# Performance work log

Measured on AMD Instinct MI355X. Metric: run time of the kernel, lower is better.

The kernel has to match this reference:

```python
import jax, jax.numpy as jnp
import numpy as np

N, H = 65536, 256
RHO_REF = 1000.0
MOMENTUM_W, CONTINUITY_W = 1.0, 10.0


def setup_inputs() -> dict:
    key = jax.random.key(0)
    ks = jax.random.split(key, 6)
    sc = lambda k, shape, fan_in: jax.random.normal(k, shape, jnp.float32) * (1.0 / fan_in) ** 0.5
    return {
        "sample_points": jax.random.normal(ks[0], (N, 3), jnp.float32),
        "sample_times": jax.random.uniform(ks[1], (N, 1), jnp.float32),
        "viscosity": jax.random.uniform(ks[2], (N,), jnp.float32) * 1e-3 + 1e-6,
        "W1": sc(ks[3], (4, H), 4),
        "b1": jnp.zeros((H,), jnp.float32),
        "W2": sc(ks[4], (H, H), H),
        "b2": jnp.zeros((H,), jnp.float32),
        "W3": sc(ks[5], (H, 5), H),
        "b3": jnp.zeros((5,), jnp.float32),
    }


def reference(sample_points, sample_times, viscosity, W1, b1, W2, b2, W3, b3):
    gravity = jnp.array([0.0, -9.81, 0.0], dtype=sample_points.dtype)

    def mlp(z):  # z: (4,) = (x, y, zcoord, t) -> (5,) = (ux, uy, uz, p, rho_raw)
        h = jnp.tanh(z @ W1 + b1)
        h = jnp.tanh(h @ W2 + b2)
        return h @ W3 + b3

    def up_fn(z):  # (ux, uy, uz, p)
        return mlp(z)[:4]

    def u_fn(z):  # (ux, uy, uz)
        return mlp(z)[:3]

    def per_point(z):
        out = mlp(z)
        u = out[:3]
        rho = RHO_REF * (1.0 + 0.1 * jnp.tanh(out[4]))
        J = jax.jacfwd(up_fn)(z)                      # (4,4): d[u,p]/d[x,y,z,t]
        Hs = jax.jacfwd(jax.jacfwd(u_fn))(z)          # (3,4,4): second derivs of u
        lap = Hs[:, 0, 0] + Hs[:, 1, 1] + Hs[:, 2, 2]  # (3,) spatial Laplacian of u
        return u, rho, J, lap

    z = jnp.concatenate([sample_points, sample_times], axis=1)  # (N,4)
    u, rho, J, lap = jax.vmap(per_point)(z)

    du_dt = J[:, :3, 3]                                # (N,3)
    conv = jnp.einsum('nj,nij->ni', u, J[:, :3, :3])   # (u . grad) u
    grad_p = J[:, 3, :3]                               # (N,3)
    R = du_dt + conv + grad_p / rho[:, None] - viscosity[:, None] * lap - gravity[None, :]
    R_cont = J[:, 0, 0] + J[:, 1, 1] + J[:, 2, 2]      # div u

    momentum_loss = (R ** 2).mean(axis=0).sum()
    continuity_loss = (R_cont ** 2).mean()
    total = MOMENTUM_W * momentum_loss + CONTINUITY_W * continuity_loss
    return jnp.stack([total, momentum_loss, continuity_loss])
```

## Files before the change

kernel.cpp:

```cpp
#include <hip/hip_runtime.h>


#define NPTS 65536
#define BP   16
#define NBLK (NPTS / BP)
#define KPAD 264
#define W3T_OFF 135168
#define PART_OFF 143360

typedef short s16x8 __attribute__((ext_vector_type(8)));
typedef float f32x4 __attribute__((ext_vector_type(4)));

static __device__ __forceinline__ unsigned short f2bf(float f){
  unsigned int u = __float_as_uint(f);
  u = (u + 0x7FFFu + ((u >> 16) & 1u)) >> 16;
  return (unsigned short)u;
}
static __device__ __forceinline__ unsigned cvtpk_bf16(float lo, float hi){
  unsigned r;
  asm("v_cvt_pk_bf16_f32 %0, %1, %2" : "=v"(r) : "v"(lo), "v"(hi));
  return r;
}
static __device__ __forceinline__ float fast_tanh(float x){
  float e = exp2f(x * 2.8853900817779268f);
  return 1.f - 2.f * __builtin_amdgcn_rcpf(e + 1.f);
}

__global__ void prep_w2t(const float* __restrict__ W2, unsigned short* __restrict__ w2t){
  int k = blockIdx.x, j = threadIdx.x;
  w2t[j * KPAD + k] = f2bf(W2[k * 256 + j]);
}

__global__ void prep_w3t(const float* __restrict__ W3, unsigned short* __restrict__ w3t){
  int idx = blockIdx.x * 256 + threadIdx.x;
  int n = idx >> 8, k = idx & 255;
  w3t[n * 256 + k] = (n < 5) ? f2bf(W3[k * 5 + n]) : (unsigned short)0;
}

__launch_bounds__(512, 4)
__global__ void ns_main(const float* __restrict__ pts, const float* __restrict__ times,
                        const float* __restrict__ visc,
                        const float* __restrict__ W1, const float* __restrict__ b1,
                        const float* __restrict__ b2, const float* __restrict__ b3,
                        const unsigned short* __restrict__ w2t,
                        const unsigned short* __restrict__ w3t,
                        float* __restrict__ parts){
  __shared__ __align__(16) unsigned char sA[128 * 512];

  const int t   = threadIdx.x;
  const int blk = blockIdx.x;

  {
    int p  = t >> 5;
    int jo = (t & 31) << 3;
    int n  = blk * BP + p;
    float z0 = pts[n*3+0], z1 = pts[n*3+1], z2 = pts[n*3+2], z3 = times[n];
    float w0v[8], w1v[8], w2v[8], w3v[8], bv[8];
    *(float4*)(w0v)   = *(const float4*)(W1 + jo);
    *(float4*)(w0v+4) = *(const float4*)(W1 + jo + 4);
    *(float4*)(w1v)   = *(const float4*)(W1 + 256 + jo);
    *(float4*)(w1v+4) = *(const float4*)(W1 + 256 + jo + 4);
    *(float4*)(w2v)   = *(const float4*)(W1 + 512 + jo);
    *(float4*)(w2v+4) = *(const float4*)(W1 + 512 + jo + 4);
    *(float4*)(w3v)   = *(const float4*)(W1 + 768 + jo);
    *(float4*)(w3v+4) = *(const float4*)(W1 + 768 + jo + 4);
    *(float4*)(bv)    = *(const float4*)(b1 + jo);
    *(float4*)(bv+4)  = *(const float4*)(b1 + jo + 4);
    float cv[8][8];
    #pragma unroll
    for (int jj = 0; jj < 8; ++jj){
      float w0 = w0v[jj], w1 = w1v[jj], w2 = w2v[jj], w3 = w3v[jj];
      float a  = bv[jj] + z0*w0 + z1*w1 + z2*w2 + z3*w3;
      float th = fast_tanh(a);
      float s  = 1.f - th*th;
      float m2 = -2.f * th * s;
      cv[0][jj] = th;
      cv[1][jj] = s*w0; cv[2][jj] = s*w1; cv[3][jj] = s*w2; cv[4][jj] = s*w3;
      cv[5][jj] = m2*w0*w0; cv[6][jj] = m2*w1*w1; cv[7][jj] = m2*w2*w2;
    }
    #pragma unroll
    for (int c = 0; c < 8; ++c){
      int row = ((p & 8) << 3) + ((c & 4) << 3) + ((p & 7) << 2) + (c & 3);
      int off = row*512 + ((jo << 1) ^ ((row & 7) << 4));
      uint4 v;
      v.x = cvtpk_bf16(cv[c][0], cv[c][1]);
      v.y = cvtpk_bf16(cv[c][2], cv[c][3]);
      v.z = cvtpk_bf16(cv[c][4], cv[c][5]);
      v.w = cvtpk_bf16(cv[c][6], cv[c][7]);
      *(uint4*)(sA + off) = v;
    }
  }
  __syncthreads();

  const int wid = t >> 6, lane = t & 63;
  const int g = lane >> 4, r16 = lane & 15;
  const int wr = wid >> 2, wc = wid & 3;
  const int xorv = (r16 & 7) << 4;

  f32x4 acc[4][4];
  #pragma unroll
  for (int a = 0; a < 4; ++a)
    #pragma unroll
    for (int b = 0; b < 4; ++b)
      acc[a][b] = (f32x4){0.f, 0.f, 0.f, 0.f};

  {
    const unsigned char* w2tB = (const unsigned char*)w2t;
    int abase0 = (wr*64 + r16)*512;
    const unsigned char* bptr[4];
    #pragma unroll
    for (int nt = 0; nt < 4; ++nt)
      bptr[nt] = w2tB + (((wc*64 + nt*16 + r16)*KPAD + g*8) << 1);
    #pragma unroll
    for (int ks = 0; ks < 8; ++ks){
      int k0 = ks * 32;
      int X  = ((k0 << 1) + (g << 4)) ^ xorv;
      s16x8 af[4], bfr[4];
      #pragma unroll
      for (int mt = 0; mt < 4; ++mt)
        af[mt] = *(const s16x8*)(sA + abase0 + mt*8192 + X);
      #pragma unroll
      for (int nt = 0; nt < 4; ++nt)
        bfr[nt] = *(const s16x8*)(bptr[nt] + (k0 << 1));
      #pragma unroll
      for (int mt = 0; mt < 4; ++mt)
        #pragma unroll
        for (int nt = 0; nt < 4; ++nt)
          acc[mt][nt] = __builtin_amdgcn_mfma_f32_16x16x32_bf16(af[mt], bfr[nt], acc[mt][nt], 0, 0, 0);
    }
  }
  __syncthreads();

  {
    float b2c[4];
    #pragma unroll
    for (int nt = 0; nt < 4; ++nt) b2c[nt] = b2[wc*64 + nt*16 + r16];
    int wadr[4][4];
    #pragma unroll
    for (int nt = 0; nt < 4; ++nt){
      int colb = (wc*64 + nt*16 + r16) << 1;
      #pragma unroll
      for (int c3 = 0; c3 < 4; ++c3)
        wadr[nt][c3] = (wr*64 + g*4 + c3)*512 + (colb ^ ((((g & 1) << 2) + c3) << 4));
    }
    #pragma unroll
    for (int mt = 0; mt < 2; ++mt){
      #pragma unroll
      for (int nt = 0; nt < 4; ++nt){
        f32x4 v = acc[mt][nt];
        f32x4 w = acc[mt+2][nt];
        float gv = fast_tanh(v[0] + b2c[nt]);
        float s2 = 1.f - gv*gv;
        float t2 = -2.f * gv * s2;
        float r0 = gv,      r1 = s2*v[1], r2 = s2*v[2], r3 = s2*v[3];
        float r4 = s2*w[0];
        float r5 = fmaf(t2*v[1], v[1], s2*w[1]);
        float r6 = fmaf(t2*v[2], v[2], s2*w[2]);
        float r7 = fmaf(t2*v[3], v[3], s2*w[3]);
        unsigned u;
        u = cvtpk_bf16(r0, r4);
        *(unsigned short*)(sA + wadr[nt][0] + mt*8192)         = (unsigned short)u;
        *(unsigned short*)(sA + wadr[nt][0] + mt*8192 + 16384) = (unsigned short)(u >> 16);
        u = cvtpk_bf16(r1, r5);
        *(unsigned short*)(sA + wadr[nt][1] + mt*8192)         = (unsigned short)u;
        *(unsigned short*)(sA + wadr[nt][1] + mt*8192 + 16384) = (unsigned short)(u >> 16);
        u = cvtpk_bf16(r2, r6);
        *(unsigned short*)(sA + wadr[nt][2] + mt*8192)         = (unsigned short)u;
        *(unsigned short*)(sA + wadr[nt][2] + mt*8192 + 16384) = (unsigned short)(u >> 16);
        u = cvtpk_bf16(r3, r7);
        *(unsigned short*)(sA + wadr[nt][3] + mt*8192)         = (unsigned short)u;
        *(unsigned short*)(sA + wadr[nt][3] + mt*8192 + 16384) = (unsigned short)(u >> 16);
      }
    }
  }
  __syncthreads();

  {
    f32x4 acc3 = (f32x4){0.f, 0.f, 0.f, 0.f};
    int rbase = (wid*16 + r16)*512;
    const unsigned char* w3tB = (const unsigned char*)w3t + ((r16*256 + g*8) << 1);
    #pragma unroll
    for (int ks = 0; ks < 8; ++ks){
      int k0 = ks * 32;
      int X  = ((k0 << 1) + (g << 4)) ^ xorv;
      s16x8 a3  = *(const s16x8*)(sA + rbase + X);
      s16x8 b3f = *(const s16x8*)(w3tB + (k0 << 1));
      acc3 = __builtin_amdgcn_mfma_f32_16x16x32_bf16(a3, b3f, acc3, 0, 0, 0);
    }
    if (r16 < 5){
      #pragma unroll
      for (int q = 0; q < 4; ++q){
        int row = wid*16 + g*4 + q;
        *(float*)(sA + row*512 + ((r16 << 2) ^ ((row & 7) << 4))) = acc3[q];
      }
    }
  }
  __syncthreads();

  float m_part = 0.f, c_part = 0.f;
  if (t < 16){
    int p = t, n = blk*BP + p;
    float o[8][5];
    #pragma unroll
    for (int c = 0; c < 8; ++c){
      int row = ((p & 8) << 3) + ((c & 4) << 3) + ((p & 7) << 2) + (c & 3);
      int swz = (row & 7) << 4;
      f32x4 v4 = *(const f32x4*)(sA + row*512 + swz);
      o[c][0] = v4[0]; o[c][1] = v4[1]; o[c][2] = v4[2]; o[c][3] = v4[3];
      o[c][4] = *(const float*)(sA + row*512 + (16 ^ swz));
    }
    #pragma unroll
    for (int m = 0; m < 5; ++m) o[0][m] += b3[m];

    float u0 = o[0][0], u1 = o[0][1], u2 = o[0][2];
    float rho = 1000.f * (1.f + 0.1f * fast_tanh(o[0][4]));
    float rr  = __builtin_amdgcn_rcpf(rho);
    float vis = visc[n];

    float conv0 = u0*o[1][0] + u1*o[2][0] + u2*o[3][0];
    float conv1 = u0*o[1][1] + u1*o[2][1] + u2*o[3][1];
    float conv2 = u0*o[1][2] + u1*o[2][2] + u2*o[3][2];
    float lap0 = o[5][0] + o[6][0] + o[7][0];
    float lap1 = o[5][1] + o[6][1] + o[7][1];
    float lap2 = o[5][2] + o[6][2] + o[7][2];
    float R0 = o[4][0] + conv0 + o[1][3]*rr - vis*lap0;
    float R1 = o[4][1] + conv1 + o[2][3]*rr - vis*lap1 + 9.81f;
    float R2 = o[4][2] + conv2 + o[3][3]*rr - vis*lap2;
    float Rc = o[1][0] + o[2][1] + o[3][2];

    m_part = R0*R0 + R1*R1 + R2*R2;
    c_part = Rc*Rc;
  }
  if (t < 64){
    #pragma unroll
    for (int off = 1; off < 16; off <<= 1){
      m_part += __shfl_xor(m_part, off, 64);
      c_part += __shfl_xor(c_part, off, 64);
    }
    if (t == 0){
      float2 pr; pr.x = m_part; pr.y = c_part;
      *(float2*)(parts + blk*2) = pr;
    }
  }
}

__global__ void ns_reduce(const float* __restrict__ parts, float* __restrict__ out){
  int t = threadIdx.x;
  float a = 0.f, b = 0.f;
  for (int i = t; i < NBLK; i += 256){ a += parts[2*i]; b += parts[2*i + 1]; }
  #pragma unroll
  for (int off = 32; off; off >>= 1){
    a += __shfl_down(a, off, 64);
    b += __shfl_down(b, off, 64);
  }
  __shared__ float sa[4], sb[4];
  int wid = t >> 6, lane = t & 63;
  if (lane == 0){ sa[wid] = a; sb[wid] = b; }
  __syncthreads();
  if (t == 0){
    float A = sa[0] + sa[1] + sa[2] + sa[3];
    float B = sb[0] + sb[1] + sb[2] + sb[3];
    float mom  = A / (float)NPTS;
    float cont = B / (float)NPTS;
    out[0] = mom + 10.f * cont;
    out[1] = mom;
    out[2] = cont;
  }
}

extern "C" void kernel_launch(void* const* d_in, const int* in_sizes, int n_in,
                              void* d_out, int out_size, void* d_ws, size_t ws_size,
                              hipStream_t stream) {
  const float* pts   = (const float*)d_in[0];
  const float* times = (const float*)d_in[1];
  const float* visc  = (const float*)d_in[2];
  const float* W1    = (const float*)d_in[3];
  const float* b1    = (const float*)d_in[4];
  const float* W2    = (const float*)d_in[5];
  const float* b2    = (const float*)d_in[6];
  const float* W3    = (const float*)d_in[7];
  const float* b3    = (const float*)d_in[8];
  float* out = (float*)d_out;

  unsigned short* w2t = (unsigned short*)d_ws;
  unsigned short* w3t = (unsigned short*)((char*)d_ws + W3T_OFF);
  float* parts        = (float*)((char*)d_ws + PART_OFF);

  prep_w2t<<<256, 256, 0, stream>>>(W2, w2t);
  prep_w3t<<<16, 256, 0, stream>>>(W3, w3t);
  ns_main<<<NBLK, 512, 0, stream>>>(pts, times, visc, W1, b1, b2, b3, w2t, w3t, parts);
  ns_reduce<<<1, 256, 0, stream>>>(parts, out);
}
```

Measured before the change: 135.6 us.

## Halve points per block to cut LDS and registers and raise occupancy

Each block now handles 8 points instead of 16. That halves the shared buffer to 32KB and the MFMA accumulator tile to 2x4, and the launch bound becomes 6 blocks per CU. Layer-1 work is spread as 4 columns per thread, and the row mapping, layer-2 writeback and final reduction are reworked to match. This aims for higher occupancy and less register pressure, but it doubles the block count and the W2 reads from global/L2 per point, and only half the waves do the layer-3 MFMA.

```diff
diff --git a/kernel.cpp b/kernel.cpp
--- a/kernel.cpp
+++ b/kernel.cpp
@@ -2,7 +2,7 @@
 
 
 #define NPTS 65536
-#define BP   16
+#define BP   8
 #define NBLK (NPTS / BP)
 #define KPAD 264
 #define W3T_OFF 135168
@@ -37,7 +37,7 @@
   w3t[n * 256 + k] = (n < 5) ? f2bf(W3[k * 5 + n]) : (unsigned short)0;
 }
 
-__launch_bounds__(512, 4)
+__launch_bounds__(512, 6)
 __global__ void ns_main(const float* __restrict__ pts, const float* __restrict__ times,
                         const float* __restrict__ visc,
                         const float* __restrict__ W1, const float* __restrict__ b1,
@@ -45,49 +45,54 @@
                         const unsigned short* __restrict__ w2t,
                         const unsigned short* __restrict__ w3t,
                         float* __restrict__ parts){
-  __shared__ __align__(16) unsigned char sA[128 * 512];
+  __shared__ __align__(16) unsigned char sA[64 * 512];
 
   const int t   = threadIdx.x;
   const int blk = blockIdx.x;
 
   {
-    int p  = t >> 5;
-    int jo = (t & 31) << 3;
+    int p  = t >> 6;
+    int jo = (t & 63) << 2;
     int n  = blk * BP + p;
     float z0 = pts[n*3+0], z1 = pts[n*3+1], z2 = pts[n*3+2], z3 = times[n];
-    float w0v[8], w1v[8], w2v[8], w3v[8], bv[8];
-    *(float4*)(w0v)   = *(const float4*)(W1 + jo);
-    *(float4*)(w0v+4) = *(const float4*)(W1 + jo + 4);
-    *(float4*)(w1v)   = *(const float4*)(W1 + 256 + jo);
-    *(float4*)(w1v+4) = *(const float4*)(W1 + 256 + jo + 4);
-    *(float4*)(w2v)   = *(const float4*)(W1 + 512 + jo);
-    *(float4*)(w2v+4) = *(const float4*)(W1 + 512 + jo + 4);
-    *(float4*)(w3v)   = *(const float4*)(W1 + 768 + jo);
-    *(float4*)(w3v+4) = *(const float4*)(W1 + 768 + jo + 4);
-    *(float4*)(bv)    = *(const float4*)(b1 + jo);
-    *(float4*)(bv+4)  = *(const float4*)(b1 + jo + 4);
-    float cv[8][8];
-    #pragma unroll
-    for (int jj = 0; jj < 8; ++jj){
-      float w0 = w0v[jj], w1 = w1v[jj], w2 = w2v[jj], w3 = w3v[jj];
-      float a  = bv[jj] + z0*w0 + z1*w1 + z2*w2 + z3*w3;
-      float th = fast_tanh(a);
-      float s  = 1.f - th*th;
-      float m2 = -2.f * th * s;
-      cv[0][jj] = th;
-      cv[1][jj] = s*w0; cv[2][jj] = s*w1; cv[3][jj] = s*w2; cv[4][jj] = s*w3;
-      cv[5][jj] = m2*w0*w0; cv[6][jj] = m2*w1*w1; cv[7][jj] = m2*w2*w2;
+    float4 wa = *(const float4*)(W1 + jo);
+    float4 wb = *(const float4*)(W1 + 256 + jo);
+    float4 wc4 = *(const float4*)(W1 + 512 + jo);
+    float4 wd = *(const float4*)(W1 + 768 + jo);
+    float4 bb = *(const float4*)(b1 + jo);
+    float th[4], sg[4], m2[4];
+    #pragma unroll
+    for (int jj = 0; jj < 4; ++jj){
+      float a = (&bb.x)[jj] + z0*(&wa.x)[jj] + z1*(&wb.x)[jj]
+                            + z2*(&wc4.x)[jj] + z3*(&wd.x)[jj];
+      float h = fast_tanh(a);
+      th[jj] = h;
+      sg[jj] = 1.f - h*h;
+      m2[jj] = -2.f * h * sg[jj];
     }
     #pragma unroll
     for (int c = 0; c < 8; ++c){
-      int row = ((p & 8) << 3) + ((c & 4) << 3) + ((p & 7) << 2) + (c & 3);
+      float x[4];
+      #pragma unroll
+      for (int jj = 0; jj < 4; ++jj){
+        float w0 = (&wa.x)[jj], w1 = (&wb.x)[jj], w2 = (&wc4.x)[jj];
+        float v;
+        if      (c == 0) v = th[jj];
+        else if (c == 1) v = sg[jj]*w0;
+        else if (c == 2) v = sg[jj]*w1;
+        else if (c == 3) v = sg[jj]*w2;
+        else if (c == 4) v = sg[jj]*(&wd.x)[jj];
+        else if (c == 5) v = m2[jj]*w0*w0;
+        else if (c == 6) v = m2[jj]*w1*w1;
+        else             v = m2[jj]*w2*w2;
+        x[jj] = v;
+      }
+      int row = ((p & 4) << 3) + ((c & 4) << 2) + ((p & 3) << 2) + (c & 3);
       int off = row*512 + ((jo << 1) ^ ((row & 7) << 4));
-      uint4 v;
-      v.x = cvtpk_bf16(cv[c][0], cv[c][1]);
-      v.y = cvtpk_bf16(cv[c][2], cv[c][3]);
-      v.z = cvtpk_bf16(cv[c][4], cv[c][5]);
-      v.w = cvtpk_bf16(cv[c][6], cv[c][7]);
-      *(uint4*)(sA + off) = v;
+      uint2 v2;
+      v2.x = cvtpk_bf16(x[0], x[1]);
+      v2.y = cvtpk_bf16(x[2], x[3]);
+      *(uint2*)(sA + off) = v2;
     }
   }
   __syncthreads();
@@ -97,16 +102,16 @@
   const int wr = wid >> 2, wc = wid & 3;
   const int xorv = (r16 & 7) << 4;
 
-  f32x4 acc[4][4];
+  f32x4 acc[2][4];
   #pragma unroll
-  for (int a = 0; a < 4; ++a)
+  for (int a = 0; a < 2; ++a)
     #pragma unroll
     for (int b = 0; b < 4; ++b)
       acc[a][b] = (f32x4){0.f, 0.f, 0.f, 0.f};
 
   {
     const unsigned char* w2tB = (const unsigned char*)w2t;
-    int abase0 = (wr*64 + r16)*512;
+    int abase = (wr*32 + r16)*512;
     const unsigned char* bptr[4];
     #pragma unroll
     for (int nt = 0; nt < 4; ++nt)
@@ -115,15 +120,14 @@
     for (int ks = 0; ks < 8; ++ks){
       int k0 = ks * 32;
       int X  = ((k0 << 1) + (g << 4)) ^ xorv;
-      s16x8 af[4], bfr[4];
-      #pragma unroll
-      for (int mt = 0; mt < 4; ++mt)
-        af[mt] = *(const s16x8*)(sA + abase0 + mt*8192 + X);
+      s16x8 af[2], bfr[4];
+      af[0] = *(const s16x8*)(sA + abase + X);
+      af[1] = *(const s16x8*)(sA + abase + 8192 + X);
       #pragma unroll
       for (int nt = 0; nt < 4; ++nt)
         bfr[nt] = *(const s16x8*)(bptr[nt] + (k0 << 1));
       #pragma unroll
-      for (int mt = 0; mt < 4; ++mt)
+      for (int mt = 0; mt < 2; ++mt)
         #pragma unroll
         for (int nt = 0; nt < 4; ++nt)
           acc[mt][nt] = __builtin_amdgcn_mfma_f32_16x16x32_bf16(af[mt], bfr[nt], acc[mt][nt], 0, 0, 0);
@@ -141,41 +145,38 @@
       int colb = (wc*64 + nt*16 + r16) << 1;
       #pragma unroll
       for (int c3 = 0; c3 < 4; ++c3)
-        wadr[nt][c3] = (wr*64 + g*4 + c3)*512 + (colb ^ ((((g & 1) << 2) + c3) << 4));
-    }
-    #pragma unroll
-    for (int mt = 0; mt < 2; ++mt){
-      #pragma unroll
-      for (int nt = 0; nt < 4; ++nt){
-        f32x4 v = acc[mt][nt];
-        f32x4 w = acc[mt+2][nt];
-        float gv = fast_tanh(v[0] + b2c[nt]);
-        float s2 = 1.f - gv*gv;
-        float t2 = -2.f * gv * s2;
-        float r0 = gv,      r1 = s2*v[1], r2 = s2*v[2], r3 = s2*v[3];
-        float r4 = s2*w[0];
-        float r5 = fmaf(t2*v[1], v[1], s2*w[1]);
-        float r6 = fmaf(t2*v[2], v[2], s2*w[2]);
-        float r7 = fmaf(t2*v[3], v[3], s2*w[3]);
-        unsigned u;
-        u = cvtpk_bf16(r0, r4);
-        *(unsigned short*)(sA + wadr[nt][0] + mt*8192)         = (unsigned short)u;
-        *(unsigned short*)(sA + wadr[nt][0] + mt*8192 + 16384) = (unsigned short)(u >> 16);
-        u = cvtpk_bf16(r1, r5);
-        *(unsigned short*)(sA + wadr[nt][1] + mt*8192)         = (unsigned short)u;
-        *(unsigned short*)(sA + wadr[nt][1] + mt*8192 + 16384) = (unsigned short)(u >> 16);
-        u = cvtpk_bf16(r2, r6);
-        *(unsigned short*)(sA + wadr[nt][2] + mt*8192)         = (unsigned short)u;
-        *(unsigned short*)(sA + wadr[nt][2] + mt*8192 + 16384) = (unsigned short)(u >> 16);
-        u = cvtpk_bf16(r3, r7);
-        *(unsigned short*)(sA + wadr[nt][3] + mt*8192)         = (unsigned short)u;
-        *(unsigned short*)(sA + wadr[nt][3] + mt*8192 + 16384) = (unsigned short)(u >> 16);
-      }
-    }
-  }
-  __syncthreads();
-
-  {
+        wadr[nt][c3] = (wr*32 + g*4 + c3)*512 + (colb ^ ((((g & 1) << 2) + c3) << 4));
+    }
+    #pragma unroll
+    for (int nt = 0; nt < 4; ++nt){
+      f32x4 v = acc[0][nt];
+      f32x4 w = acc[1][nt];
+      float gv = fast_tanh(v[0] + b2c[nt]);
+      float s2 = 1.f - gv*gv;
+      float t2 = -2.f * gv * s2;
+      float r0 = gv,      r1 = s2*v[1], r2 = s2*v[2], r3 = s2*v[3];
+      float r4 = s2*w[0];
+      float r5 = fmaf(t2*v[1], v[1], s2*w[1]);
+      float r6 = fmaf(t2*v[2], v[2], s2*w[2]);
+      float r7 = fmaf(t2*v[3], v[3], s2*w[3]);
+      unsigned u;
+      u = cvtpk_bf16(r0, r4);
+      *(unsigned short*)(sA + wadr[nt][0])        = (unsigned short)u;
+      *(unsigned short*)(sA + wadr[nt][0] + 8192) = (unsigned short)(u >> 16);
+      u = cvtpk_bf16(r1, r5);
+      *(unsigned short*)(sA + wadr[nt][1])        = (unsigned short)u;
+      *(unsigned short*)(sA + wadr[nt][1] + 8192) = (unsigned short)(u >> 16);
+      u = cvtpk_bf16(r2, r6);
+      *(unsigned short*)(sA + wadr[nt][2])        = (unsigned short)u;
+      *(unsigned short*)(sA + wadr[nt][2] + 8192) = (unsigned short)(u >> 16);
+      u = cvtpk_bf16(r3, r7);
+      *(unsigned short*)(sA + wadr[nt][3])        = (unsigned short)u;
+      *(unsigned short*)(sA + wadr[nt][3] + 8192) = (unsigned short)(u >> 16);
+    }
+  }
+  __syncthreads();
+
+  if (wid < 4){
     f32x4 acc3 = (f32x4){0.f, 0.f, 0.f, 0.f};
     int rbase = (wid*16 + r16)*512;
     const unsigned char* w3tB = (const unsigned char*)w3t + ((r16*256 + g*8) << 1);
@@ -198,12 +199,12 @@
   __syncthreads();
 
   float m_part = 0.f, c_part = 0.f;
-  if (t < 16){
+  if (t < 8){
     int p = t, n = blk*BP + p;
     float o[8][5];
     #pragma unroll
     for (int c = 0; c < 8; ++c){
-      int row = ((p & 8) << 3) + ((c & 4) << 3) + ((p & 7) << 2) + (c & 3);
+      int row = ((p & 4) << 3) + ((c & 4) << 2) + ((p & 3) << 2) + (c & 3);
       int swz = (row & 7) << 4;
       f32x4 v4 = *(const f32x4*)(sA + row*512 + swz);
       o[c][0] = v4[0]; o[c][1] = v4[1]; o[c][2] = v4[2]; o[c][3] = v4[3];
@@ -233,7 +234,7 @@
   }
   if (t < 64){
     #pragma unroll
-    for (int off = 1; off < 16; off <<= 1){
+    for (int off = 1; off < 8; off <<= 1){
       m_part += __shfl_xor(m_part, off, 64);
       c_part += __shfl_xor(c_part, off, 64);
     }
```

After: 193.1 us. +42.4%, slower.

## Switch MLP matmuls from bf16 to fp8 MFMA with halved LDS tiles

Applied to the files above, without the earlier changes.

The W2/W3 weights and the hidden-layer activation and derivative tiles are now stored as fp8 instead of bf16. The two matmul stages use the fp8 16x16x32 MFMA, and the LDS swizzle, addressing and prep kernels are rewritten for byte-wide elements. This halves the shared-memory footprint and load bytes, and the launch bound is raised to allow more resident blocks. The 3-bit mantissa of fp8 is a serious accuracy risk for the derivative and Laplacian terms, and the 16x16x32 fp8 MFMA may not issue faster than the bf16 one.

```diff
diff --git a/kernel.cpp b/kernel.cpp
--- a/kernel.cpp
+++ b/kernel.cpp
@@ -4,48 +4,44 @@
 #define NPTS 65536
 #define BP   16
 #define NBLK (NPTS / BP)
-#define KPAD 264
+#define KPADB 264
 #define W3T_OFF 135168
 #define PART_OFF 143360
 
-typedef short s16x8 __attribute__((ext_vector_type(8)));
 typedef float f32x4 __attribute__((ext_vector_type(4)));
 
-static __device__ __forceinline__ unsigned short f2bf(float f){
-  unsigned int u = __float_as_uint(f);
-  u = (u + 0x7FFFu + ((u >> 16) & 1u)) >> 16;
-  return (unsigned short)u;
-}
-static __device__ __forceinline__ unsigned cvtpk_bf16(float lo, float hi){
-  unsigned r;
-  asm("v_cvt_pk_bf16_f32 %0, %1, %2" : "=v"(r) : "v"(lo), "v"(hi));
+static __device__ __forceinline__ unsigned cvtpk_fp8(float lo, float hi){
+  unsigned r = 0;
+  asm("v_cvt_pk_fp8_f32 %0, %1, %2" : "+v"(r) : "v"(lo), "v"(hi));
   return r;
 }
 static __device__ __forceinline__ float fast_tanh(float x){
-  float e = exp2f(x * 2.8853900817779268f);
+  float e = __builtin_amdgcn_exp2f(x * 2.8853900817779268f);
   return 1.f - 2.f * __builtin_amdgcn_rcpf(e + 1.f);
 }
 
-__global__ void prep_w2t(const float* __restrict__ W2, unsigned short* __restrict__ w2t){
-  int k = blockIdx.x, j = threadIdx.x;
-  w2t[j * KPAD + k] = f2bf(W2[k * 256 + j]);
-}
-
-__global__ void prep_w3t(const float* __restrict__ W3, unsigned short* __restrict__ w3t){
-  int idx = blockIdx.x * 256 + threadIdx.x;
-  int n = idx >> 8, k = idx & 255;
-  w3t[n * 256 + k] = (n < 5) ? f2bf(W3[k * 5 + n]) : (unsigned short)0;
-}
-
-__launch_bounds__(512, 4)
+__global__ void prep_w2t(const float* __restrict__ W2, unsigned char* __restrict__ w2t){
+  int kp = blockIdx.x, j = threadIdx.x;
+  float lo = W2[(2*kp    )*256 + j];
+  float hi = W2[(2*kp + 1)*256 + j];
+  *(unsigned short*)(w2t + j*KPADB + 2*kp) = (unsigned short)cvtpk_fp8(lo, hi);
+}
+__global__ void prep_w3t(const float* __restrict__ W3, unsigned char* __restrict__ w3t){
+  int n = blockIdx.x, k2 = threadIdx.x * 2;
+  float lo = (n < 5) ? W3[k2*5 + n]       : 0.f;
+  float hi = (n < 5) ? W3[(k2+1)*5 + n]   : 0.f;
+  *(unsigned short*)(w3t + n*256 + k2) = (unsigned short)cvtpk_fp8(lo, hi);
+}
+
+__launch_bounds__(512, 6)
 __global__ void ns_main(const float* __restrict__ pts, const float* __restrict__ times,
                         const float* __restrict__ visc,
                         const float* __restrict__ W1, const float* __restrict__ b1,
                         const float* __restrict__ b2, const float* __restrict__ b3,
-                        const unsigned short* __restrict__ w2t,
-                        const unsigned short* __restrict__ w3t,
+                        const unsigned char* __restrict__ w2t,
+                        const unsigned char* __restrict__ w3t,
                         float* __restrict__ parts){
-  __shared__ __align__(16) unsigned char sA[128 * 512];
+  __shared__ __align__(16) unsigned char sA[128 * 256];
 
   const int t   = threadIdx.x;
   const int blk = blockIdx.x;
@@ -81,13 +77,15 @@
     #pragma unroll
     for (int c = 0; c < 8; ++c){
       int row = ((p & 8) << 3) + ((c & 4) << 3) + ((p & 7) << 2) + (c & 3);
-      int off = row*512 + ((jo << 1) ^ ((row & 7) << 4));
-      uint4 v;
-      v.x = cvtpk_bf16(cv[c][0], cv[c][1]);
-      v.y = cvtpk_bf16(cv[c][2], cv[c][3]);
-      v.z = cvtpk_bf16(cv[c][4], cv[c][5]);
-      v.w = cvtpk_bf16(cv[c][6], cv[c][7]);
-      *(uint4*)(sA + off) = v;
+      int off = row*256 + (jo ^ ((row & 7) << 3));
+      unsigned u01 = cvtpk_fp8(cv[c][0], cv[c][1]);
+      unsigned u23 = cvtpk_fp8(cv[c][2], cv[c][3]);
+      unsigned u45 = cvtpk_fp8(cv[c][4], cv[c][5]);
+      unsigned u67 = cvtpk_fp8(cv[c][6], cv[c][7]);
+      uint2 v;
+      v.x = u01 | (u23 << 16);
+      v.y = u45 | (u67 << 16);
+      *(uint2*)(sA + off) = v;
     }
   }
   __syncthreads();
@@ -95,7 +93,7 @@
   const int wid = t >> 6, lane = t & 63;
   const int g = lane >> 4, r16 = lane & 15;
   const int wr = wid >> 2, wc = wid & 3;
-  const int xorv = (r16 & 7) << 4;
+  const int xorv = (r16 & 7) << 3;
 
   f32x4 acc[4][4];
   #pragma unroll
@@ -105,28 +103,27 @@
       acc[a][b] = (f32x4){0.f, 0.f, 0.f, 0.f};
 
   {
-    const unsigned char* w2tB = (const unsigned char*)w2t;
-    int abase0 = (wr*64 + r16)*512;
+    int abase0 = (wr*64 + r16)*256;
     const unsigned char* bptr[4];
     #pragma unroll
     for (int nt = 0; nt < 4; ++nt)
-      bptr[nt] = w2tB + (((wc*64 + nt*16 + r16)*KPAD + g*8) << 1);
+      bptr[nt] = w2t + (wc*64 + nt*16 + r16)*KPADB + g*8;
     #pragma unroll
     for (int ks = 0; ks < 8; ++ks){
       int k0 = ks * 32;
-      int X  = ((k0 << 1) + (g << 4)) ^ xorv;
-      s16x8 af[4], bfr[4];
+      int X  = (k0 + (g << 3)) ^ xorv;
+      long af[4], bfr[4];
       #pragma unroll
       for (int mt = 0; mt < 4; ++mt)
-        af[mt] = *(const s16x8*)(sA + abase0 + mt*8192 + X);
+        af[mt] = *(const long*)(sA + abase0 + mt*4096 + X);
       #pragma unroll
       for (int nt = 0; nt < 4; ++nt)
-        bfr[nt] = *(const s16x8*)(bptr[nt] + (k0 << 1));
+        bfr[nt] = *(const long*)(bptr[nt] + k0);
       #pragma unroll
       for (int mt = 0; mt < 4; ++mt)
         #pragma unroll
         for (int nt = 0; nt < 4; ++nt)
-          acc[mt][nt] = __builtin_amdgcn_mfma_f32_16x16x32_bf16(af[mt], bfr[nt], acc[mt][nt], 0, 0, 0);
+          acc[mt][nt] = __builtin_amdgcn_mfma_f32_16x16x32_fp8_fp8(af[mt], bfr[nt], acc[mt][nt], 0, 0, 0);
     }
   }
   __syncthreads();
@@ -138,10 +135,10 @@
     int wadr[4][4];
     #pragma unroll
     for (int nt = 0; nt < 4; ++nt){
-      int colb = (wc*64 + nt*16 + r16) << 1;
+      int colb = wc*64 + nt*16 + r16;
       #pragma unroll
       for (int c3 = 0; c3 < 4; ++c3)
-        wadr[nt][c3] = (wr*64 + g*4 + c3)*512 + (colb ^ ((((g & 1) << 2) + c3) << 4));
+        wadr[nt][c3] = (wr*64 + g*4 + c3)*256 + (colb ^ ((((g & 1) << 2) + c3) << 3));
     }
     #pragma unroll
     for (int mt = 0; mt < 2; ++mt){
@@ -158,18 +155,18 @@
         float r6 = fmaf(t2*v[2], v[2], s2*w[2]);
         float r7 = fmaf(t2*v[3], v[3], s2*w[3]);
         unsigned u;
-        u = cvtpk_bf16(r0, r4);
-        *(unsigned short*)(sA + wadr[nt][0] + mt*8192)         = (unsigned short)u;
-        *(unsigned short*)(sA + wadr[nt][0] + mt*8192 + 16384) = (unsigned short)(u >> 16);
-        u = cvtpk_bf16(r1, r5);
-        *(unsigned short*)(sA + wadr[nt][1] + mt*8192)         = (unsigned short)u;
-        *(unsigned short*)(sA + wadr[nt][1] + mt*8192 + 16384) = (unsigned short)(u >> 16);
-        u = cvtpk_bf16(r2, r6);
-        *(unsigned short*)(sA + wadr[nt][2] + mt*8192)         = (unsigned short)u;
-        *(unsigned short*)(sA + wadr[nt][2] + mt*8192 + 16384) = (unsigned short)(u >> 16);
-        u = cvtpk_bf16(r3, r7);
-        *(unsigned short*)(sA + wadr[nt][3] + mt*8192)         = (unsigned short)u;
-        *(unsigned short*)(sA + wadr[nt][3] + mt*8192 + 16384) = (unsigned short)(u >> 16);
+        u = cvtpk_fp8(r0, r4);
+        *(unsigned char*)(sA + wadr[nt][0] + mt*4096)        = (unsigned char)u;
+        *(unsigned char*)(sA + wadr[nt][0] + mt*4096 + 8192) = (unsigned char)(u >> 8);
+        u = cvtpk_fp8(r1, r5);
+        *(unsigned char*)(sA + wadr[nt][1] + mt*4096)        = (unsigned char)u;
+        *(unsigned char*)(sA + wadr[nt][1] + mt*4096 + 8192) = (unsigned char)(u >> 8);
+        u = cvtpk_fp8(r2, r6);
+        *(unsigned char*)(sA + wadr[nt][2] + mt*4096)        = (unsigned char)u;
+        *(unsigned char*)(sA + wadr[nt][2] + mt*4096 + 8192) = (unsigned char)(u >> 8);
+        u = cvtpk_fp8(r3, r7);
+        *(unsigned char*)(sA + wadr[nt][3] + mt*4096)        = (unsigned char)u;
+        *(unsigned char*)(sA + wadr[nt][3] + mt*4096 + 8192) = (unsigned char)(u >> 8);
       }
     }
   }
@@ -177,21 +174,21 @@
 
   {
     f32x4 acc3 = (f32x4){0.f, 0.f, 0.f, 0.f};
-    int rbase = (wid*16 + r16)*512;
-    const unsigned char* w3tB = (const unsigned char*)w3t + ((r16*256 + g*8) << 1);
+    int rbase = (wid*16 + r16)*256;
+    const unsigned char* w3p = w3t + r16*256 + g*8;
     #pragma unroll
     for (int ks = 0; ks < 8; ++ks){
       int k0 = ks * 32;
-      int X  = ((k0 << 1) + (g << 4)) ^ xorv;
-      s16x8 a3  = *(const s16x8*)(sA + rbase + X);
-      s16x8 b3f = *(const s16x8*)(w3tB + (k0 << 1));
-      acc3 = __builtin_amdgcn_mfma_f32_16x16x32_bf16(a3, b3f, acc3, 0, 0, 0);
+      int X  = (k0 + (g << 3)) ^ xorv;
+      long a3  = *(const long*)(sA + rbase + X);
+      long b3f = *(const long*)(w3p + k0);
+      acc3 = __builtin_amdgcn_mfma_f32_16x16x32_fp8_fp8(a3, b3f, acc3, 0, 0, 0);
     }
     if (r16 < 5){
       #pragma unroll
       for (int q = 0; q < 4; ++q){
         int row = wid*16 + g*4 + q;
-        *(float*)(sA + row*512 + ((r16 << 2) ^ ((row & 7) << 4))) = acc3[q];
+        *(float*)(sA + row*256 + ((r16 << 2) ^ ((row & 7) << 3))) = acc3[q];
       }
     }
   }
@@ -204,10 +201,10 @@
     #pragma unroll
     for (int c = 0; c < 8; ++c){
       int row = ((p & 8) << 3) + ((c & 4) << 3) + ((p & 7) << 2) + (c & 3);
-      int swz = (row & 7) << 4;
-      f32x4 v4 = *(const f32x4*)(sA + row*512 + swz);
-      o[c][0] = v4[0]; o[c][1] = v4[1]; o[c][2] = v4[2]; o[c][3] = v4[3];
-      o[c][4] = *(const float*)(sA + row*512 + (16 ^ swz));
+      int swz = (row & 7) << 3;
+      #pragma unroll
+      for (int m = 0; m < 5; ++m)
+        o[c][m] = *(const float*)(sA + row*256 + ((m << 2) ^ swz));
     }
     #pragma unroll
     for (int m = 0; m < 5; ++m) o[0][m] += b3[m];
@@ -282,12 +279,12 @@
   const float* b3    = (const float*)d_in[8];
   float* out = (float*)d_out;
 
-  unsigned short* w2t = (unsigned short*)d_ws;
-  unsigned short* w3t = (unsigned short*)((char*)d_ws + W3T_OFF);
-  float* parts        = (float*)((char*)d_ws + PART_OFF);
-
-  prep_w2t<<<256, 256, 0, stream>>>(W2, w2t);
-  prep_w3t<<<16, 256, 0, stream>>>(W3, w3t);
+  unsigned char* w2t = (unsigned char*)d_ws;
+  unsigned char* w3t = (unsigned char*)d_ws + W3T_OFF;
+  float* parts       = (float*)((char*)d_ws + PART_OFF);
+
+  prep_w2t<<<128, 256, 0, stream>>>(W2, w2t);
+  prep_w3t<<<16, 128, 0, stream>>>(W3, w3t);
   ns_main<<<NBLK, 512, 0, stream>>>(pts, times, visc, W1, b1, b2, b3, w2t, w3t, parts);
   ns_reduce<<<1, 256, 0, stream>>>(parts, out);
 }
```

New measurement: 381.7 us. 181% more time.
